# Kernel optimization log

Hardware: AMD Instinct MI355X
Metric: run time of the kernel (lower is better)

## Reference

```python
import jax, jax.numpy as jnp
from jax import lax
import numpy as np

# H=W=16 is forced by the module: mask path is a fixed 4x4 lowres map -> ConvTranspose(stride 4) -> 16x16
B, T, H, W = 512, 18, 16, 16
CH, K, D = 128, 8, 128


def setup_inputs():
    key = jax.random.key(0)
    ks = iter(jax.random.split(key, 40))
    def rn(shape, s=0.1):
        return jax.random.normal(next(ks), shape, jnp.float32) * s
    return dict(
        frames=jax.random.uniform(next(ks), (B, T, 1, H, W), jnp.float32),
        enc1_w=rn((CH, 2, 3, 3)), enc1_b=rn((CH,)),
        enc2_w=rn((CH, CH, 4, 4), 0.02), enc2_b=rn((CH,)),
        slot_mu=rn((1, K, D), 0.1),
        to_slot_w=rn((D, CH)), to_slot_b=rn((D,)),
        q_w=rn((D, D)), k_w=rn((D, D)), v_w=rn((D, D)),
        gru_w_ih=rn((3 * D, D)), gru_w_hh=rn((3 * D, D)),
        gru_b_ih=rn((3 * D,)), gru_b_hh=rn((3 * D,)),
        mot1_w=rn((32, D)), mot1_b=rn((32,)),
        mot2_w=rn((2, 32)), mot2_b=rn((2,)),
        mask_w=rn((CH * 16, D)), mask_b=rn((CH * 16,)),
        up_w=rn((K, K, 4, 4)), up_b=rn((K,)),
        res1_w=rn((CH // 2, 1, 3, 3)), res1_b=rn((CH // 2,)),
        res2_w=rn((1, CH // 2, 3, 3)), res2_b=rn((1,)),
    )


def _conv(x, w, b, stride, pad):
    y = lax.conv_general_dilated(x, w, (stride, stride), [(pad, pad), (pad, pad)],
                                 dimension_numbers=('NCHW', 'OIHW', 'NCHW'))
    return y + b[None, :, None, None]


def _gelu(x):
    return jax.nn.gelu(x, approximate=False)  # torch nn.GELU default = exact erf


def reference(frames, enc1_w, enc1_b, enc2_w, enc2_b, slot_mu, to_slot_w, to_slot_b,
              q_w, k_w, v_w, gru_w_ih, gru_w_hh, gru_b_ih, gru_b_hh,
              mot1_w, mot1_b, mot2_w, mot2_b, mask_w, mask_b, up_w, up_b,
              res1_w, res1_b, res2_w, res2_b):
    Bq, Tq = frames.shape[0], frames.shape[1]
    Hh, Ww = frames.shape[-2], frames.shape[-1]
    Kq, Dq = slot_mu.shape[1], slot_mu.shape[2]
    scale = Dq ** 0.5
    # base sampling grid in normalized [-1,1] coords, order (x, y)
    gy, gx = jnp.meshgrid(jnp.linspace(-1.0, 1.0, Hh), jnp.linspace(-1.0, 1.0, Ww), indexing='ij')
    grid = jnp.stack([gx, gy], axis=-1)  # [H,W,2]
    # ConvTranspose2d weight [in,out,kh,kw] -> equivalent forward-conv kernel (swap io, flip spatial)
    up_w_f = jnp.flip(up_w, (2, 3)).transpose(1, 0, 2, 3)

    def gru(x, h):  # torch nn.GRUCell, gate order r,z,n
        gi = x @ gru_w_ih.T + gru_b_ih
        gh = h @ gru_w_hh.T + gru_b_hh
        ir, iz, inn = jnp.split(gi, 3, axis=-1)
        hr, hz, hn = jnp.split(gh, 3, axis=-1)
        r = jax.nn.sigmoid(ir + hr)
        z = jax.nn.sigmoid(iz + hz)
        n = jnp.tanh(inn + r * hn)
        return (1.0 - z) * n + z * h

    def step(slots, pair):
        curr = pair[:, :1]  # [B,1,H,W]
        feat = _gelu(_conv(pair, enc1_w, enc1_b, 1, 1))
        feat = _gelu(_conv(feat, enc2_w, enc2_b, 4, 0))  # [B,CH,H/4,W/4]
        fs = jnp.einsum('bcn,dc->bnd', feat.reshape(Bq, feat.shape[1], -1), to_slot_w) + to_slot_b
        kk = fs @ k_w.T
        vv = fs @ v_w.T
        for _ in range(3):  # fixed 3 slot-attention iterations
            qq = slots @ q_w.T
            attn = jax.nn.softmax(jnp.einsum('bkd,bnd->bkn', qq, kk) / scale, axis=1)
            upd = jnp.einsum('bkn,bnd->bkd', attn, vv)
            slots = gru(upd.reshape(-1, Dq), slots.reshape(-1, Dq)).reshape(Bq, Kq, Dq)
        motion = jnp.tanh(_gelu(slots @ mot1_w.T + mot1_b) @ mot2_w.T + mot2_b) * 4.0  # [B,K,2]
        ml = (slots @ mask_w.T + mask_b).reshape(Bq, Kq, -1, 4, 4).mean(axis=2)  # [B,K,4,4]
        masks = lax.conv_general_dilated(ml, up_w_f, (1, 1), [(3, 3), (3, 3)],
                                         lhs_dilation=(4, 4),
                                         dimension_numbers=('NCHW', 'OIHW', 'NCHW')) + up_b[None, :, None, None]
        masks = jax.nn.softmax(masks, axis=1)  # [B,K,16,16]
        # batched per-slot warp (constant translation per slot); grid_sample bilinear,
        # border padding, align_corners=True
        fsc = motion * 2.0 / jnp.array([Ww, Hh], jnp.float32)
        sg = jnp.clip(grid[None, None] + fsc[:, :, None, None, :], -1.0, 1.0)  # [B,K,H,W,2]
        ix = (sg[..., 0] + 1.0) * 0.5 * (Ww - 1)
        iy = (sg[..., 1] + 1.0) * 0.5 * (Hh - 1)
        x0 = jnp.floor(ix); y0 = jnp.floor(iy)
        wx = ix - x0; wy = iy - y0
        x0i = jnp.clip(x0, 0, Ww - 1).astype(jnp.int32)
        x1i = jnp.clip(x0 + 1, 0, Ww - 1).astype(jnp.int32)
        y0i = jnp.clip(y0, 0, Hh - 1).astype(jnp.int32)
        y1i = jnp.clip(y0 + 1, 0, Hh - 1).astype(jnp.int32)
        img = curr[:, 0]  # [B,H,W]
        bidx = jnp.arange(Bq)[:, None, None, None]
        v00 = img[bidx, y0i, x0i]; v01 = img[bidx, y0i, x1i]
        v10 = img[bidx, y1i, x0i]; v11 = img[bidx, y1i, x1i]
        warped_k = (1 - wy) * ((1 - wx) * v00 + wx * v01) + wy * ((1 - wx) * v10 + wx * v11)  # [B,K,H,W]
        warped = (masks * warped_k).sum(axis=1, keepdims=True)  # [B,1,H,W]
        res = jnp.tanh(_conv(_gelu(_conv(warped - curr, res1_w, res1_b, 1, 1)), res2_w, res2_b, 1, 1)) * 0.1
        pred = jnp.clip(warped + res, 0.0, 1.0)
        return slots, pred

    slots0 = jnp.broadcast_to(slot_mu, (Bq, Kq, Dq))
    # pair = cat([curr, prev], dim=1) for t in 0..T-3
    pairs = jnp.swapaxes(jnp.concatenate([frames[:, 1:Tq - 1], frames[:, :Tq - 2]], axis=2), 0, 1)
    _, preds = lax.scan(step, slots0, pairs)
    return jnp.swapaxes(preds, 0, 1)  # [B,T-2,1,H,W]
```

## Files before the change

kernel.cpp:

```cpp
#include <hip/hip_runtime.h>
#include <math.h>

#define B_TOT 512
#define T_FR  18
#define NSTEP 16

typedef __attribute__((ext_vector_type(8))) short bf16x8;
typedef __attribute__((ext_vector_type(4))) float f32x4;

__device__ __forceinline__ float gelu_f(float x) {
    return 0.5f * x * (1.0f + erff(x * 0.70710678118654752f));
}
__device__ __forceinline__ float sigmoid_f(float x) {
    return 1.0f / (1.0f + expf(-x));
}
__device__ __forceinline__ short f2bf(float x) {
    unsigned int u = __float_as_uint(x);
    return (short)((u + 0x7FFFu + ((u >> 16) & 1u)) >> 16);
}
__device__ __forceinline__ float bflo(unsigned int u) { return __uint_as_float(u << 16); }
__device__ __forceinline__ float bfhi(unsigned int u) { return __uint_as_float(u & 0xffff0000u); }
__device__ __forceinline__ float bf2f(short s) {
    return __uint_as_float(((unsigned int)(unsigned short)s) << 16);
}
__device__ __forceinline__ bf16x8 ld_bf8(const short* p) {
    const short4 lo = *reinterpret_cast<const short4*>(p);
    const short4 hi = *reinterpret_cast<const short4*>(p + 4);
    bf16x8 r;
    r[0] = lo.x; r[1] = lo.y; r[2] = lo.z; r[3] = lo.w;
    r[4] = hi.x; r[5] = hi.y; r[6] = hi.z; r[7] = hi.w;
    return r;
}

#define MFMA(a, bb, c) __builtin_amdgcn_mfma_f32_16x16x32_bf16((a), (bb), (c), 0, 0, 0)

__global__ __launch_bounds__(256) void init_kernel(
    const float* __restrict__ mask_w, const float* __restrict__ mask_b,
    const float* __restrict__ e2w,
    const float* __restrict__ wih, const float* __restrict__ whh,
    const float* __restrict__ qw,
    const float* __restrict__ tsw, const float* __restrict__ tsb,
    const float* __restrict__ kw, const float* __restrict__ vw,
    const float* __restrict__ e1w, const float* __restrict__ e1b,
    float* __restrict__ rmw, float* __restrict__ rmb,
    float* __restrict__ kbf, float* __restrict__ vbf,
    short* __restrict__ w2bf, short* __restrict__ wihbf, short* __restrict__ whhbf,
    short* __restrict__ qwbf, short* __restrict__ kwf, short* __restrict__ vwf,
    short* __restrict__ e1wbf)
{
    const int tid = threadIdx.x, bid = blockIdx.x;
    const int gid = bid * 256 + tid, gstr = gridDim.x * 256;
    const float rscale = 0.08838834764831845f;

    for (int i = gid; i < 128 * 2048; i += gstr) w2bf[i] = f2bf(e2w[i]);
    for (int i = gid; i < 384 * 128; i += gstr) {
        wihbf[i] = f2bf(wih[i]);
        whhbf[i] = f2bf(whh[i]);
    }
    for (int i = gid; i < 128 * 128; i += gstr) qwbf[i] = f2bf(qw[i] * rscale);
    for (int i = gid; i < 128 * 32; i += gstr) {
        const int ci = i >> 5, k = i & 31;
        float v = 0.f;
        if (k < 18) v = e1w[ci * 18 + k];
        else if (k == 18) v = e1b[ci];
        e1wbf[i] = f2bf(v);
    }

    if (bid < 128) {
        const int j = bid;
        if (tid < 128) {
            float s = 0.f;
            for (int d = 0; d < 128; ++d) s += kw[j * 128 + d] * tsw[d * 128 + tid];
            kwf[j * 128 + tid] = f2bf(s);
        } else if (tid == 128) {
            float s = 0.f;
            for (int d = 0; d < 128; ++d) s += kw[j * 128 + d] * tsb[d];
            kbf[j] = s;
        }
    } else if (bid < 256) {
        const int j = bid - 128;
        if (tid < 128) {
            float s = 0.f;
            for (int d = 0; d < 128; ++d) s += vw[j * 128 + d] * tsw[d * 128 + tid];
            vwf[j * 128 + tid] = f2bf(s);
        } else if (tid == 128) {
            float s = 0.f;
            for (int d = 0; d < 128; ++d) s += vw[j * 128 + d] * tsb[d];
            vbf[j] = s;
        }
    }
    if (bid == 256) {
        for (int i = tid; i < 2048; i += 256) {
            const int j = i >> 7, d = i & 127;
            float s = 0.f;
            for (int c = 0; c < 128; ++c) s += mask_w[(c * 16 + j) * 128 + d];
            rmw[i] = s * (1.0f / 128.0f);
        }
        for (int i = tid; i < 16; i += 256) {
            float s = 0.f;
            for (int c = 0; c < 128; ++c) s += mask_b[c * 16 + i];
            rmb[i] = s * (1.0f / 128.0f);
        }
    }
}

#define E_PAIR 0
#define E_IM2C 2048
#define E_F1S  20480
#define E_F2T  40960
#define E_E2B  45184
#define E_KBF  45696
#define E_VBF  46208
#define EPOOLSZ 46720

__global__ __launch_bounds__(256, 2) void encoder_all_kernel(
    const float* __restrict__ frames,
    const short* __restrict__ w2bf, const short* __restrict__ e1wbf,
    const float* __restrict__ e2b_g,
    const short* __restrict__ kwf, const short* __restrict__ vwf,
    const float* __restrict__ kbf_g, const float* __restrict__ vbf_g,
    short* __restrict__ kk_g, short* __restrict__ vv_g)
{
    __shared__ __align__(16) char POOL[EPOOLSZ];
    float* PAIR = (float*)(POOL + E_PAIR);
    short* IM2C = (short*)(POOL + E_IM2C);
    short* F1S  = (short*)(POOL + E_F1S);
    short* F2T  = (short*)(POOL + E_F2T);
    float* E2B  = (float*)(POOL + E_E2B);
    float* KBF  = (float*)(POOL + E_KBF);
    float* VBF  = (float*)(POOL + E_VBF);

    const int tid = threadIdx.x;
    const int lane = tid & 63, w = tid >> 6;
    const int g = lane >> 4, cn = lane & 15;
    const int bid = blockIdx.x;
    const int b = bid >> 4, t = bid & 15;
    const int py = tid >> 4, pxx = tid & 15;
    const int arow = (2 * w) * 16 + cn;
    const int bcol = (4 * (cn >> 2) + (g & 1) * 2) * 20 + 4 * (cn & 3);

    PAIR[tid]       = frames[((size_t)b * T_FR + t + 1) * 256 + tid];
    PAIR[256 + tid] = frames[((size_t)b * T_FR + t) * 256 + tid];
    if (tid < 128) {
        E2B[tid] = e2b_g[tid];
        KBF[tid] = kbf_g[tid];
        VBF[tid] = vbf_g[tid];
    }
    __syncthreads();

    {
        short* imr = &IM2C[tid * 36];
#pragma unroll
        for (int ky = 0; ky < 3; ++ky)
#pragma unroll
        for (int kx = 0; kx < 3; ++kx) {
            const int yy = py + ky - 1, xx = pxx + kx - 1;
            const bool ok = (yy >= 0 && yy < 16 && xx >= 0 && xx < 16);
            const int q = ky * 3 + kx;
            imr[q]     = ok ? f2bf(PAIR[yy * 16 + xx]) : (short)0;
            imr[9 + q] = ok ? f2bf(PAIR[256 + yy * 16 + xx]) : (short)0;
        }
        imr[18] = (short)0x3F80;
        imr[19] = 0;
        short4 z4; z4.x = 0; z4.y = 0; z4.z = 0; z4.w = 0;
        *(short4*)&imr[20] = z4;
        *(short4*)&imr[24] = z4;
        *(short4*)&imr[28] = z4;
    }
    __syncthreads();

    f32x4 acc0 = {0.f, 0.f, 0.f, 0.f};
    f32x4 acc1 = {0.f, 0.f, 0.f, 0.f};
    for (int ch = 0; ch < 4; ++ch) {
        {
            const bf16x8 aw0 = *(const bf16x8*)&e1wbf[(size_t)(ch * 32 + cn) * 32 + g * 8];
            const bf16x8 aw1 = *(const bf16x8*)&e1wbf[(size_t)(ch * 32 + 16 + cn) * 32 + g * 8];
            f32x4 c0[4], c1[4];
#pragma unroll
            for (int j = 0; j < 4; ++j) {
                c0[j] = (f32x4){0.f, 0.f, 0.f, 0.f};
                c1[j] = (f32x4){0.f, 0.f, 0.f, 0.f};
            }
#pragma unroll
            for (int j = 0; j < 4; ++j) {
                const int pos = (4 * w + j) * 16 + cn;
                const bf16x8 bim = ld_bf8(&IM2C[pos * 36 + g * 8]);
                c0[j] = MFMA(aw0, bim, c0[j]);
                c1[j] = MFMA(aw1, bim, c1[j]);
            }
#pragma unroll
            for (int j = 0; j < 4; ++j)
#pragma unroll
            for (int r = 0; r < 4; ++r) {
                F1S[(4 * g + r) * 320 + (4 * w + j) * 20 + cn] = f2bf(gelu_f(c0[j][r]));
                F1S[(16 + 4 * g + r) * 320 + (4 * w + j) * 20 + cn] = f2bf(gelu_f(c1[j][r]));
            }
        }
        __syncthreads();
        int rb = (g >> 1) * 320 + bcol;
        int k0 = ch * 512 + g * 8;
        for (int kt = 0; kt < 16; ++kt) {
            const short4 lo = *(const short4*)&F1S[rb];
            const short4 hi = *(const short4*)&F1S[rb + 20];
            bf16x8 bfr;
            bfr[0] = lo.x; bfr[1] = lo.y; bfr[2] = lo.z; bfr[3] = lo.w;
            bfr[4] = hi.x; bfr[5] = hi.y; bfr[6] = hi.z; bfr[7] = hi.w;
            const bf16x8 a0 = *(const bf16x8*)&w2bf[(size_t)arow * 2048 + k0];
            const bf16x8 a1 = *(const bf16x8*)&w2bf[(size_t)(arow + 16) * 2048 + k0];
            acc0 = MFMA(a0, bfr, acc0);
            acc1 = MFMA(a1, bfr, acc1);
            rb += 640; k0 += 32;
        }
        __syncthreads();
    }
    {
        const int cob0 = (2 * w) * 16 + g * 4;
        short4 s0, s1;
        s0.x = f2bf(gelu_f(acc0[0] + E2B[cob0]));
        s0.y = f2bf(gelu_f(acc0[1] + E2B[cob0 + 1]));
        s0.z = f2bf(gelu_f(acc0[2] + E2B[cob0 + 2]));
        s0.w = f2bf(gelu_f(acc0[3] + E2B[cob0 + 3]));
        s1.x = f2bf(gelu_f(acc1[0] + E2B[cob0 + 16]));
        s1.y = f2bf(gelu_f(acc1[1] + E2B[cob0 + 17]));
        s1.z = f2bf(gelu_f(acc1[2] + E2B[cob0 + 18]));
        s1.w = f2bf(gelu_f(acc1[3] + E2B[cob0 + 19]));
        *(short4*)&F2T[cn * 132 + cob0] = s0;
        *(short4*)&F2T[cn * 132 + cob0 + 16] = s1;
    }
    __syncthreads();

    {
        bf16x8 aT[4];
#pragma unroll
        for (int kt = 0; kt < 4; ++kt)
            aT[kt] = ld_bf8(&F2T[cn * 132 + kt * 32 + g * 8]);
        const short* wf = (w >> 1) ? vwf : kwf;
        const int h2 = w & 1;
        f32x4 ac[4];
#pragma unroll
        for (int nt = 0; nt < 4; ++nt) ac[nt] = (f32x4){0.f, 0.f, 0.f, 0.f};
#pragma unroll
        for (int kt = 0; kt < 4; ++kt)
#pragma unroll
        for (int nt = 0; nt < 4; ++nt)
            ac[nt] = MFMA(aT[kt],
                *(const bf16x8*)&wf[(size_t)(h2 * 64 + nt * 16 + cn) * 128 + kt * 32 + g * 8],
                ac[nt]);
        short* dst = (w >> 1) ? vv_g : kk_g;
        const float* bias = (w >> 1) ? VBF : KBF;
        const size_t base = (size_t)bid * 2048;
#pragma unroll
        for (int nt = 0; nt < 4; ++nt) {
            const int j = h2 * 64 + nt * 16 + cn;
            const float bb = bias[j];
#pragma unroll
            for (int r = 0; r < 4; ++r)
                dst[base + (4 * g + r) * 128 + j] = f2bf(ac[nt][r] + bb);
        }
    }
}

#define PO_BIH   0
#define PO_BHH   1536
#define PO_M1B   3072
#define PO_M2W   3200
#define PO_M2B   3456
#define PO_UPB   3472
#define PO_RMB   3504
#define PO_R2B   3568
#define PO_UPW   3584
#define PO_R1W   7680
#define PO_R1B   9984
#define PO_R2W   10240
#define PO_M1W   12544
#define PO_RMW   20992
#define PO_SLOTS 25216
#define PO_SLB   29312
#define SCR2     33536
#define T_KK   0
#define T_VV   4224
#define T_QQ   8448
#define T_UPD  12672
#define T_ATT  16896
#define T_MASK 0
#define T_IMG  8192
#define T_WARP 9216
#define T_DIFF 10240
#define T_M1O  11264
#define T_MOT  12288
#define T_MLL  12416
#define T_R1S  12928
#define POOLSZ2 (33536 + 21376)

#define LDW(mat, row, kt) (*(const bf16x8*)&mat[(size_t)(row) * 128 + (kt) * 32 + g * 8])

__global__ __launch_bounds__(256, 2) void fused_seq_kernel(
    const float* __restrict__ frames,
    const float* __restrict__ slot_mu,
    const short* __restrict__ kk_g, const short* __restrict__ vv_g,
    const short* __restrict__ qwbf,
    const short* __restrict__ wihbf, const short* __restrict__ whhbf,
    const float* __restrict__ bih_g, const float* __restrict__ bhh_g,
    const float* __restrict__ m1w_g, const float* __restrict__ m1b_g,
    const float* __restrict__ m2w_g, const float* __restrict__ m2b_g,
    const float* __restrict__ upw_g, const float* __restrict__ upb_g,
    const float* __restrict__ r1w_g, const float* __restrict__ r1b_g,
    const float* __restrict__ r2w_g, const float* __restrict__ r2b_g,
    const float* __restrict__ rmw_g, const float* __restrict__ rmb_g,
    float* __restrict__ out)
{
    __shared__ __align__(16) char POOL[POOLSZ2];
    const int tid = threadIdx.x;
    const int lane = tid & 63, w = tid >> 6;
    const int g = lane >> 4, cn = lane & 15;
    const int b = blockIdx.x;

    float* BIH = (float*)(POOL + PO_BIH);
    float* BHH = (float*)(POOL + PO_BHH);
    float* M1B = (float*)(POOL + PO_M1B);
    float* M2W = (float*)(POOL + PO_M2W);
    float* M2B = (float*)(POOL + PO_M2B);
    float* UPB = (float*)(POOL + PO_UPB);
    float* RMB = (float*)(POOL + PO_RMB);
    float* R2B = (float*)(POOL + PO_R2B);
    float* UPW = (float*)(POOL + PO_UPW);
    float* R1W = (float*)(POOL + PO_R1W);
    float* R1B = (float*)(POOL + PO_R1B);
    float* R2W = (float*)(POOL + PO_R2W);
    short* M1W = (short*)(POOL + PO_M1W);
    short* RMW = (short*)(POOL + PO_RMW);
    float* SLOTS = (float*)(POOL + PO_SLOTS);
    short* SLB = (short*)(POOL + PO_SLB);

    short* KKl  = (short*)(POOL + SCR2 + T_KK);
    short* VVl  = (short*)(POOL + SCR2 + T_VV);
    short* QQB  = (short*)(POOL + SCR2 + T_QQ);
    short* UPDB = (short*)(POOL + SCR2 + T_UPD);
    float* ATT  = (float*)(POOL + SCR2 + T_ATT);
    float* MASKl = (float*)(POOL + SCR2 + T_MASK);
    float* IMG  = (float*)(POOL + SCR2 + T_IMG);
    float* WARP = (float*)(POOL + SCR2 + T_WARP);
    float* DIFF = (float*)(POOL + SCR2 + T_DIFF);
    float* M1O  = (float*)(POOL + SCR2 + T_M1O);
    float* MOT  = (float*)(POOL + SCR2 + T_MOT);
    float* MLL  = (float*)(POOL + SCR2 + T_MLL);
    short* R1S  = (short*)(POOL + SCR2 + T_R1S);

    for (int i = tid; i < 384; i += 256) { BIH[i] = bih_g[i]; BHH[i] = bhh_g[i]; }
    if (tid < 32) M1B[tid] = m1b_g[tid];
    if (tid < 64) { M2W[tid] = m2w_g[tid]; R1B[tid] = r1b_g[tid]; }
    if (tid < 2) M2B[tid] = m2b_g[tid];
    if (tid < 8) UPB[tid] = upb_g[tid];
    if (tid < 16) RMB[tid] = rmb_g[tid];
    if (tid == 0) R2B[0] = r2b_g[0];
    for (int i = tid; i < 1024; i += 256) UPW[i] = upw_g[i];
    for (int i = tid; i < 576; i += 256) { R1W[i] = r1w_g[i]; R2W[i] = r2w_g[i]; }
    for (int i = tid; i < 4096; i += 256)
        M1W[(i >> 7) * 132 + (i & 127)] = f2bf(m1w_g[i]);
    for (int i = tid; i < 2048; i += 256)
        RMW[(i >> 7) * 132 + (i & 127)] = f2bf(rmw_g[i]);
    for (int i = tid; i < 1024; i += 256) {
        const float v = slot_mu[i];
        SLOTS[i] = v;
        SLB[(i >> 7) * 132 + (i & 127)] = f2bf(v);
    }
    for (int i = tid; i < 8 * 132; i += 256) SLB[8 * 132 + i] = 0;

    const int col0 = 32 * w;
    const int py = tid >> 4, pxx = tid & 15;
    __syncthreads();

#pragma unroll 1
    for (int t = 0; t < NSTEP; ++t) {
        const float imgv = frames[((size_t)b * T_FR + t + 1) * 256 + tid];

        {
            const size_t base = ((size_t)b * 16 + t) * 2048;
            const int row = tid >> 4, c8 = (tid & 15) * 8;
            const short4 klo = *(const short4*)&kk_g[base + row * 128 + c8];
            const short4 khi = *(const short4*)&kk_g[base + row * 128 + c8 + 4];
            const short4 vlo = *(const short4*)&vv_g[base + row * 128 + c8];
            const short4 vhi = *(const short4*)&vv_g[base + row * 128 + c8 + 4];
            *(short4*)&KKl[row * 132 + c8] = klo;
            *(short4*)&KKl[row * 132 + c8 + 4] = khi;
            *(short4*)&VVl[row * 132 + c8] = vlo;
            *(short4*)&VVl[row * 132 + c8 + 4] = vhi;
        }
        __syncthreads();

        for (int it = 0; it < 3; ++it) {
            bf16x8 aS[4];
#pragma unroll
            for (int kt = 0; kt < 4; ++kt)
                aS[kt] = ld_bf8(&SLB[cn * 132 + kt * 32 + g * 8]);
            {
                f32x4 qa[2] = {{0.f, 0.f, 0.f, 0.f}, {0.f, 0.f, 0.f, 0.f}};
#pragma unroll
                for (int kt = 0; kt < 4; ++kt)
#pragma unroll
                for (int nt = 0; nt < 2; ++nt)
                    qa[nt] = MFMA(aS[kt], LDW(qwbf, col0 + nt * 16 + cn, kt), qa[nt]);
#pragma unroll
                for (int nt = 0; nt < 2; ++nt)
#pragma unroll
                for (int r = 0; r < 4; ++r)
                    QQB[(4 * g + r) * 132 + col0 + nt * 16 + cn] = f2bf(qa[nt][r]);
            }
            __syncthreads();
            if (tid < 128) {
                const int n = tid >> 3, k = tid & 7;
                float a = 0.f;
                for (int d = 0; d < 128; d += 4) {
                    const uint2 q2 = *(const uint2*)&QQB[k * 132 + d];
                    const uint2 k2 = *(const uint2*)&KKl[n * 132 + d];
                    a += bflo(q2.x) * bflo(k2.x) + bfhi(q2.x) * bfhi(k2.x)
                       + bflo(q2.y) * bflo(k2.y) + bfhi(q2.y) * bfhi(k2.y);
                }
                float m = a;
                m = fmaxf(m, __shfl_xor(m, 1));
                m = fmaxf(m, __shfl_xor(m, 2));
                m = fmaxf(m, __shfl_xor(m, 4));
                const float e = expf(a - m);
                float s = e;
                s += __shfl_xor(s, 1);
                s += __shfl_xor(s, 2);
                s += __shfl_xor(s, 4);
                ATT[k * 16 + n] = e / s;
            }
            __syncthreads();
            {
                const int k8 = tid >> 5, lg = tid & 31;
                float a0 = 0.f, a1 = 0.f, a2 = 0.f, a3 = 0.f;
#pragma unroll
                for (int n = 0; n < 16; ++n) {
                    const float at = ATT[k8 * 16 + n];
                    const uint2 v2 = *(const uint2*)&VVl[n * 132 + 4 * lg];
                    a0 += at * bflo(v2.x); a1 += at * bfhi(v2.x);
                    a2 += at * bflo(v2.y); a3 += at * bfhi(v2.y);
                }
                short4 sv;
                sv.x = f2bf(a0); sv.y = f2bf(a1); sv.z = f2bf(a2); sv.w = f2bf(a3);
                *(short4*)&UPDB[k8 * 132 + 4 * lg] = sv;
            }
            __syncthreads();
            {
                bf16x8 aU[4];
#pragma unroll
                for (int kt = 0; kt < 4; ++kt)
                    aU[kt] = ld_bf8(&UPDB[cn * 132 + kt * 32 + g * 8]);
                f32x4 aR[2], aZ[2], aNIv[2], aNHv[2];
#pragma unroll
                for (int nt = 0; nt < 2; ++nt) {
                    aR[nt] = (f32x4){0.f, 0.f, 0.f, 0.f};
                    aZ[nt] = (f32x4){0.f, 0.f, 0.f, 0.f};
                    aNIv[nt] = (f32x4){0.f, 0.f, 0.f, 0.f};
                    aNHv[nt] = (f32x4){0.f, 0.f, 0.f, 0.f};
                }
#pragma unroll
                for (int nt = 0; nt < 2; ++nt) {
                    const int colj = col0 + nt * 16 + cn;
#pragma unroll
                    for (int kt = 0; kt < 4; ++kt) {
                        aR[nt]   = MFMA(aU[kt], LDW(wihbf, colj, kt), aR[nt]);
                        aR[nt]   = MFMA(aS[kt], LDW(whhbf, colj, kt), aR[nt]);
                        aZ[nt]   = MFMA(aU[kt], LDW(wihbf, 128 + colj, kt), aZ[nt]);
                        aZ[nt]   = MFMA(aS[kt], LDW(whhbf, 128 + colj, kt), aZ[nt]);
                        aNIv[nt] = MFMA(aU[kt], LDW(wihbf, 256 + colj, kt), aNIv[nt]);
                        aNHv[nt] = MFMA(aS[kt], LDW(whhbf, 256 + colj, kt), aNHv[nt]);
                    }
                }
                __syncthreads();
                if (g < 2) {
#pragma unroll
                    for (int nt = 0; nt < 2; ++nt) {
                        const int colj = col0 + nt * 16 + cn;
                        const float br = BIH[colj] + BHH[colj];
                        const float bz = BIH[128 + colj] + BHH[128 + colj];
                        const float bi = BIH[256 + colj], bh = BHH[256 + colj];
#pragma unroll
                        for (int r = 0; r < 4; ++r) {
                            const int kq = 4 * g + r;
                            const float rr = sigmoid_f(aR[nt][r] + br);
                            const float zz = sigmoid_f(aZ[nt][r] + bz);
                            const float nn = tanhf(aNIv[nt][r] + bi + rr * (aNHv[nt][r] + bh));
                            const float hold = SLOTS[kq * 128 + colj];
                            const float hv = (1.f - zz) * nn + zz * hold;
                            SLOTS[kq * 128 + colj] = hv;
                            SLB[kq * 132 + colj] = f2bf(hv);
                        }
                    }
                }
                __syncthreads();
            }
        }

        IMG[tid] = imgv;
        {
            const int kq = tid >> 5, c = tid & 31;
            float a = M1B[c];
            for (int d = 0; d < 128; d += 4) {
                const uint2 s2 = *(const uint2*)&SLB[kq * 132 + d];
                const uint2 w2 = *(const uint2*)&M1W[c * 132 + d];
                a += bflo(s2.x) * bflo(w2.x) + bfhi(s2.x) * bfhi(w2.x)
                   + bflo(s2.y) * bflo(w2.y) + bfhi(s2.y) * bfhi(w2.y);
            }
            M1O[kq * 32 + c] = gelu_f(a);
        }
        if (tid < 128) {
            const int kq = tid >> 4, j = tid & 15;
            float a = RMB[j];
            for (int d = 0; d < 128; d += 4) {
                const uint2 s2 = *(const uint2*)&SLB[kq * 132 + d];
                const uint2 w2 = *(const uint2*)&RMW[j * 132 + d];
                a += bflo(s2.x) * bflo(w2.x) + bfhi(s2.x) * bfhi(w2.x)
                   + bflo(s2.y) * bflo(w2.y) + bfhi(s2.y) * bfhi(w2.y);
            }
            MLL[kq * 16 + j] = a;
        }
        __syncthreads();
        if (tid < 16) {
            const int kq = tid >> 1, e = tid & 1;
            float a = M2B[e];
#pragma unroll
            for (int c = 0; c < 32; ++c) a += M1O[kq * 32 + c] * M2W[e * 32 + c];
            MOT[kq * 2 + e] = tanhf(a) * 4.0f;
        }
        {
            const int jj = (py >> 2) * 4 + (pxx >> 2);
            const int wq = (py & 3) * 4 + (pxx & 3);
#pragma unroll
            for (int ko = 0; ko < 8; ++ko) {
                float a = UPB[ko];
#pragma unroll
                for (int i8 = 0; i8 < 8; ++i8)
                    a += MLL[i8 * 16 + jj] * UPW[(i8 * 8 + ko) * 16 + wq];
                MASKl[ko * 256 + tid] = a;
            }
        }
        __syncthreads();
        {
            float m = -1e30f;
#pragma unroll
            for (int kq = 0; kq < 8; ++kq) m = fmaxf(m, MASKl[kq * 256 + tid]);
            float e[8], ssum = 0.f;
#pragma unroll
            for (int kq = 0; kq < 8; ++kq) { e[kq] = expf(MASKl[kq * 256 + tid] - m); ssum += e[kq]; }
            const float inv = 1.f / ssum;
            const float gxv = -1.0f + (2.0f / 15.0f) * pxx;
            const float gyv = -1.0f + (2.0f / 15.0f) * py;
            float wsum = 0.f;
#pragma unroll
            for (int kq = 0; kq < 8; ++kq) {
                const float fx = MOT[kq * 2 + 0] * 0.125f;
                const float fy = MOT[kq * 2 + 1] * 0.125f;
                const float sgx = fminf(fmaxf(gxv + fx, -1.f), 1.f);
                const float sgy = fminf(fmaxf(gyv + fy, -1.f), 1.f);
                const float ix = (sgx + 1.f) * 7.5f;
                const float iy = (sgy + 1.f) * 7.5f;
                const float x0f = floorf(ix), y0f = floorf(iy);
                const float wx = ix - x0f, wy = iy - y0f;
                const int x0 = (int)x0f, y0 = (int)y0f;
                const int x1 = min(x0 + 1, 15), y1 = min(y0 + 1, 15);
                const float v00 = IMG[y0 * 16 + x0], v01 = IMG[y0 * 16 + x1];
                const float v10 = IMG[y1 * 16 + x0], v11 = IMG[y1 * 16 + x1];
                const float val = (1.f - wy) * ((1.f - wx) * v00 + wx * v01) +
                                  wy * ((1.f - wx) * v10 + wx * v11);
                wsum += (e[kq] * inv) * val;
            }
            WARP[tid] = wsum;
            DIFF[tid] = wsum - IMG[tid];
        }
        __syncthreads();
        float nbz[9];
#pragma unroll
        for (int ky = 0; ky < 3; ++ky)
#pragma unroll
        for (int kx = 0; kx < 3; ++kx) {
            const int y2 = py + ky - 1, x2 = pxx + kx - 1;
            const bool ok = (y2 >= 0 && y2 < 16 && x2 >= 0 && x2 < 16);
            nbz[ky * 3 + kx] = ok ? DIFF[y2 * 16 + x2] : 0.f;
        }
        float racc = 0.f;
        for (int c0 = 0; c0 < 64; c0 += 16) {
#pragma unroll 4
            for (int cl = 0; cl < 16; ++cl) {
                const int c = c0 + cl;
                float a = R1B[c];
#pragma unroll
                for (int q = 0; q < 9; ++q) a += nbz[q] * R1W[c * 9 + q];
                R1S[cl * 264 + tid] = f2bf(gelu_f(a));
            }
            __syncthreads();
#pragma unroll 4
            for (int cl = 0; cl < 16; ++cl) {
                const float* r2r = &R2W[(c0 + cl) * 9];
#pragma unroll
                for (int ky = 0; ky < 3; ++ky)
#pragma unroll
                for (int kx = 0; kx < 3; ++kx) {
                    const int y2 = py + ky - 1, x2 = pxx + kx - 1;
                    if (y2 >= 0 && y2 < 16 && x2 >= 0 && x2 < 16)
                        racc += bf2f(R1S[cl * 264 + y2 * 16 + x2]) * r2r[ky * 3 + kx];
                }
            }
            __syncthreads();
        }
        const float resv = tanhf(racc + R2B[0]) * 0.1f;
        const float pred = fminf(fmaxf(WARP[tid] + resv, 0.f), 1.f);
        out[((size_t)b * NSTEP + t) * 256 + tid] = pred;
        __syncthreads();
    }
}

extern "C" void kernel_launch(void* const* d_in, const int* in_sizes, int n_in,
                              void* d_out, int out_size, void* d_ws, size_t ws_size,
                              hipStream_t stream)
{
    const float* frames = (const float*)d_in[0];
    const float* e1w = (const float*)d_in[1];
    const float* e1b = (const float*)d_in[2];
    const float* e2w = (const float*)d_in[3];
    const float* e2b = (const float*)d_in[4];
    const float* slot_mu = (const float*)d_in[5];
    const float* tsw = (const float*)d_in[6];
    const float* tsb = (const float*)d_in[7];
    const float* qw = (const float*)d_in[8];
    const float* kw = (const float*)d_in[9];
    const float* vw = (const float*)d_in[10];
    const float* wih = (const float*)d_in[11];
    const float* whh = (const float*)d_in[12];
    const float* bih = (const float*)d_in[13];
    const float* bhh = (const float*)d_in[14];
    const float* m1w = (const float*)d_in[15];
    const float* m1b = (const float*)d_in[16];
    const float* m2w = (const float*)d_in[17];
    const float* m2b = (const float*)d_in[18];
    const float* maskw = (const float*)d_in[19];
    const float* maskb = (const float*)d_in[20];
    const float* upw = (const float*)d_in[21];
    const float* upb = (const float*)d_in[22];
    const float* r1w = (const float*)d_in[23];
    const float* r1b = (const float*)d_in[24];
    const float* r2w = (const float*)d_in[25];
    const float* r2b = (const float*)d_in[26];

    float* ws = (float*)d_ws;
    float* rmw  = ws + 0;
    float* rmb  = ws + 2048;
    float* kbf  = ws + 2064;
    float* vbf  = ws + 2192;
    short* w2bf  = (short*)(ws + 2320);
    short* wihbf = (short*)(ws + 133392);
    short* whhbf = (short*)(ws + 157968);
    short* qwbf  = (short*)(ws + 182544);
    short* kwf   = (short*)(ws + 190736);
    short* vwf   = (short*)(ws + 198928);
    short* e1wbf = (short*)(ws + 207120);
    short* kk_g  = (short*)(ws + 209168);
    short* vv_g  = (short*)(ws + 209168 + 8388608);

    hipLaunchKernelGGL(init_kernel, dim3(512), dim3(256), 0, stream,
                       maskw, maskb, e2w, wih, whh, qw, tsw, tsb, kw, vw,
                       e1w, e1b,
                       rmw, rmb, kbf, vbf, w2bf, wihbf, whhbf, qwbf, kwf, vwf,
                       e1wbf);
    hipLaunchKernelGGL(encoder_all_kernel, dim3(B_TOT * NSTEP), dim3(256), 0, stream,
                       frames, w2bf, e1wbf, e2b, kwf, vwf, kbf, vbf, kk_g, vv_g);
    hipLaunchKernelGGL(fused_seq_kernel, dim3(B_TOT), dim3(256), 0, stream,
                       frames, slot_mu, kk_g, vv_g, qwbf, wihbf, whhbf, bih, bhh,
                       m1w, m1b, m2w, m2b, upw, upb,
                       r1w, r1b, r2w, r2b, rmw, rmb,
                       (float*)d_out);
}
```

Before: 1.803 ms.

## Split per-step decoder out of sequential slot kernel into parallel decode kernel

The slot recurrence kernel no longer runs the motion/mask/warp/residual decoder inside its time loop. It writes the updated slots for each step into the kk_g buffer, overwriting the K values already consumed for that step. A new kernel with one block per (batch, step) then runs the decoder, so decode work no longer sits on the 512-block sequential critical path and its shared memory leaves the recurrent kernel, which may allow more occupancy. The cost is an extra launch, a global round trip of the slots, and reloading the decoder weights in every one of 8192 blocks.

```diff
diff --git a/kernel.cpp b/kernel.cpp
--- a/kernel.cpp
+++ b/kernel.cpp
@@ -262,52 +262,24 @@
 
 #define PO_BIH   0
 #define PO_BHH   1536
-#define PO_M1B   3072
-#define PO_M2W   3200
-#define PO_M2B   3456
-#define PO_UPB   3472
-#define PO_RMB   3504
-#define PO_R2B   3568
-#define PO_UPW   3584
-#define PO_R1W   7680
-#define PO_R1B   9984
-#define PO_R2W   10240
-#define PO_M1W   12544
-#define PO_RMW   20992
-#define PO_SLOTS 25216
-#define PO_SLB   29312
-#define SCR2     33536
+#define PO_SLOTS 3072
+#define PO_SLB   7168
+#define SCR2     11392
 #define T_KK   0
 #define T_VV   4224
 #define T_QQ   8448
 #define T_UPD  12672
 #define T_ATT  16896
-#define T_MASK 0
-#define T_IMG  8192
-#define T_WARP 9216
-#define T_DIFF 10240
-#define T_M1O  11264
-#define T_MOT  12288
-#define T_MLL  12416
-#define T_R1S  12928
-#define POOLSZ2 (33536 + 21376)
+#define POOLSZ2 (11392 + 17408)
 
 #define LDW(mat, row, kt) (*(const bf16x8*)&mat[(size_t)(row) * 128 + (kt) * 32 + g * 8])
 
 __global__ __launch_bounds__(256, 2) void fused_seq_kernel(
-    const float* __restrict__ frames,
     const float* __restrict__ slot_mu,
-    const short* __restrict__ kk_g, const short* __restrict__ vv_g,
+    short* __restrict__ kk_g, const short* __restrict__ vv_g,
     const short* __restrict__ qwbf,
     const short* __restrict__ wihbf, const short* __restrict__ whhbf,
-    const float* __restrict__ bih_g, const float* __restrict__ bhh_g,
-    const float* __restrict__ m1w_g, const float* __restrict__ m1b_g,
-    const float* __restrict__ m2w_g, const float* __restrict__ m2b_g,
-    const float* __restrict__ upw_g, const float* __restrict__ upb_g,
-    const float* __restrict__ r1w_g, const float* __restrict__ r1b_g,
-    const float* __restrict__ r2w_g, const float* __restrict__ r2b_g,
-    const float* __restrict__ rmw_g, const float* __restrict__ rmb_g,
-    float* __restrict__ out)
+    const float* __restrict__ bih_g, const float* __restrict__ bhh_g)
 {
     __shared__ __align__(16) char POOL[POOLSZ2];
     const int tid = threadIdx.x;
@@ -317,18 +289,6 @@
 
     float* BIH = (float*)(POOL + PO_BIH);
     float* BHH = (float*)(POOL + PO_BHH);
-    float* M1B = (float*)(POOL + PO_M1B);
-    float* M2W = (float*)(POOL + PO_M2W);
-    float* M2B = (float*)(POOL + PO_M2B);
-    float* UPB = (float*)(POOL + PO_UPB);
-    float* RMB = (float*)(POOL + PO_RMB);
-    float* R2B = (float*)(POOL + PO_R2B);
-    float* UPW = (float*)(POOL + PO_UPW);
-    float* R1W = (float*)(POOL + PO_R1W);
-    float* R1B = (float*)(POOL + PO_R1B);
-    float* R2W = (float*)(POOL + PO_R2W);
-    short* M1W = (short*)(POOL + PO_M1W);
-    short* RMW = (short*)(POOL + PO_RMW);
     float* SLOTS = (float*)(POOL + PO_SLOTS);
     short* SLB = (short*)(POOL + PO_SLB);
 
@@ -337,28 +297,8 @@
     short* QQB  = (short*)(POOL + SCR2 + T_QQ);
     short* UPDB = (short*)(POOL + SCR2 + T_UPD);
     float* ATT  = (float*)(POOL + SCR2 + T_ATT);
-    float* MASKl = (float*)(POOL + SCR2 + T_MASK);
-    float* IMG  = (float*)(POOL + SCR2 + T_IMG);
-    float* WARP = (float*)(POOL + SCR2 + T_WARP);
-    float* DIFF = (float*)(POOL + SCR2 + T_DIFF);
-    float* M1O  = (float*)(POOL + SCR2 + T_M1O);
-    float* MOT  = (float*)(POOL + SCR2 + T_MOT);
-    float* MLL  = (float*)(POOL + SCR2 + T_MLL);
-    short* R1S  = (short*)(POOL + SCR2 + T_R1S);
 
     for (int i = tid; i < 384; i += 256) { BIH[i] = bih_g[i]; BHH[i] = bhh_g[i]; }
-    if (tid < 32) M1B[tid] = m1b_g[tid];
-    if (tid < 64) { M2W[tid] = m2w_g[tid]; R1B[tid] = r1b_g[tid]; }
-    if (tid < 2) M2B[tid] = m2b_g[tid];
-    if (tid < 8) UPB[tid] = upb_g[tid];
-    if (tid < 16) RMB[tid] = rmb_g[tid];
-    if (tid == 0) R2B[0] = r2b_g[0];
-    for (int i = tid; i < 1024; i += 256) UPW[i] = upw_g[i];
-    for (int i = tid; i < 576; i += 256) { R1W[i] = r1w_g[i]; R2W[i] = r2w_g[i]; }
-    for (int i = tid; i < 4096; i += 256)
-        M1W[(i >> 7) * 132 + (i & 127)] = f2bf(m1w_g[i]);
-    for (int i = tid; i < 2048; i += 256)
-        RMW[(i >> 7) * 132 + (i & 127)] = f2bf(rmw_g[i]);
     for (int i = tid; i < 1024; i += 256) {
         const float v = slot_mu[i];
         SLOTS[i] = v;
@@ -367,13 +307,10 @@
     for (int i = tid; i < 8 * 132; i += 256) SLB[8 * 132 + i] = 0;
 
     const int col0 = 32 * w;
-    const int py = tid >> 4, pxx = tid & 15;
     __syncthreads();
 
 #pragma unroll 1
     for (int t = 0; t < NSTEP; ++t) {
-        const float imgv = frames[((size_t)b * T_FR + t + 1) * 256 + tid];
-
         {
             const size_t base = ((size_t)b * 16 + t) * 2048;
             const int row = tid >> 4, c8 = (tid & 15) * 8;
@@ -494,122 +431,212 @@
             }
         }
 
-        IMG[tid] = imgv;
         {
-            const int kq = tid >> 5, c = tid & 31;
-            float a = M1B[c];
-            for (int d = 0; d < 128; d += 4) {
-                const uint2 s2 = *(const uint2*)&SLB[kq * 132 + d];
-                const uint2 w2 = *(const uint2*)&M1W[c * 132 + d];
-                a += bflo(s2.x) * bflo(w2.x) + bfhi(s2.x) * bfhi(w2.x)
-                   + bflo(s2.y) * bflo(w2.y) + bfhi(s2.y) * bfhi(w2.y);
+            const size_t base = ((size_t)b * 16 + t) * 2048;
+            const int i4 = tid * 4;
+            const int row = i4 >> 7, col = i4 & 127;
+            *(short4*)&kk_g[base + i4] = *(const short4*)&SLB[row * 132 + col];
+        }
+        __syncthreads();
+    }
+}
+
+#define D_SLB  0
+#define D_M1W  2112
+#define D_RMW  10560
+#define D_UPW  14784
+#define D_R1W  18880
+#define D_R2W  21184
+#define D_M1B  23488
+#define D_M2W  23616
+#define D_M2B  23872
+#define D_UPB  23888
+#define D_RMB  23920
+#define D_R2B  23984
+#define D_R1B  24000
+#define D_IMG  24256
+#define D_MASK 25280
+#define D_WARP 33472
+#define D_DIFF 34496
+#define D_M1O  35520
+#define D_MOT  36544
+#define D_MLL  36672
+#define D_R1S  37184
+#define POOLSZ3 45632
+
+__global__ __launch_bounds__(256, 2) void decode_all_kernel(
+    const float* __restrict__ frames,
+    const short* __restrict__ slots_g,
+    const float* __restrict__ m1w_g, const float* __restrict__ m1b_g,
+    const float* __restrict__ m2w_g, const float* __restrict__ m2b_g,
+    const float* __restrict__ upw_g, const float* __restrict__ upb_g,
+    const float* __restrict__ r1w_g, const float* __restrict__ r1b_g,
+    const float* __restrict__ r2w_g, const float* __restrict__ r2b_g,
+    const float* __restrict__ rmw_g, const float* __restrict__ rmb_g,
+    float* __restrict__ out)
+{
+    __shared__ __align__(16) char POOL[POOLSZ3];
+    short* SLB = (short*)(POOL + D_SLB);
+    short* M1W = (short*)(POOL + D_M1W);
+    short* RMW = (short*)(POOL + D_RMW);
+    float* UPW = (float*)(POOL + D_UPW);
+    float* R1W = (float*)(POOL + D_R1W);
+    float* R2W = (float*)(POOL + D_R2W);
+    float* M1B = (float*)(POOL + D_M1B);
+    float* M2W = (float*)(POOL + D_M2W);
+    float* M2B = (float*)(POOL + D_M2B);
+    float* UPB = (float*)(POOL + D_UPB);
+    float* RMB = (float*)(POOL + D_RMB);
+    float* R2B = (float*)(POOL + D_R2B);
+    float* R1B = (float*)(POOL + D_R1B);
+    float* IMG = (float*)(POOL + D_IMG);
+    float* MASKl = (float*)(POOL + D_MASK);
+    float* WARP = (float*)(POOL + D_WARP);
+    float* DIFF = (float*)(POOL + D_DIFF);
+    float* M1O  = (float*)(POOL + D_M1O);
+    float* MOT  = (float*)(POOL + D_MOT);
+    float* MLL  = (float*)(POOL + D_MLL);
+    short* R1S  = (short*)(POOL + D_R1S);
+
+    const int tid = threadIdx.x;
+    const int bid = blockIdx.x;
+    const int b = bid >> 4, t = bid & 15;
+    const int py = tid >> 4, pxx = tid & 15;
+
+    {
+        const size_t base = (size_t)bid * 2048;
+        const int i4 = tid * 4;
+        const int row = i4 >> 7, col = i4 & 127;
+        *(short4*)&SLB[row * 132 + col] = *(const short4*)&slots_g[base + i4];
+    }
+    for (int i = tid; i < 4096; i += 256)
+        M1W[(i >> 7) * 132 + (i & 127)] = f2bf(m1w_g[i]);
+    for (int i = tid; i < 2048; i += 256)
+        RMW[(i >> 7) * 132 + (i & 127)] = f2bf(rmw_g[i]);
+    for (int i = tid; i < 1024; i += 256) UPW[i] = upw_g[i];
+    for (int i = tid; i < 576; i += 256) { R1W[i] = r1w_g[i]; R2W[i] = r2w_g[i]; }
+    if (tid < 32) M1B[tid] = m1b_g[tid];
+    if (tid < 64) { M2W[tid] = m2w_g[tid]; R1B[tid] = r1b_g[tid]; }
+    if (tid < 2) M2B[tid] = m2b_g[tid];
+    if (tid < 8) UPB[tid] = upb_g[tid];
+    if (tid < 16) RMB[tid] = rmb_g[tid];
+    if (tid == 0) R2B[0] = r2b_g[0];
+    IMG[tid] = frames[((size_t)b * T_FR + t + 1) * 256 + tid];
+    __syncthreads();
+
+    {
+        const int kq = tid >> 5, c = tid & 31;
+        float a = M1B[c];
+        for (int d = 0; d < 128; d += 4) {
+            const uint2 s2 = *(const uint2*)&SLB[kq * 132 + d];
+            const uint2 w2 = *(const uint2*)&M1W[c * 132 + d];
+            a += bflo(s2.x) * bflo(w2.x) + bfhi(s2.x) * bfhi(w2.x)
+               + bflo(s2.y) * bflo(w2.y) + bfhi(s2.y) * bfhi(w2.y);
+        }
+        M1O[kq * 32 + c] = gelu_f(a);
+    }
+    if (tid < 128) {
+        const int kq = tid >> 4, j = tid & 15;
+        float a = RMB[j];
+        for (int d = 0; d < 128; d += 4) {
+            const uint2 s2 = *(const uint2*)&SLB[kq * 132 + d];
+            const uint2 w2 = *(const uint2*)&RMW[j * 132 + d];
+            a += bflo(s2.x) * bflo(w2.x) + bfhi(s2.x) * bfhi(w2.x)
+               + bflo(s2.y) * bflo(w2.y) + bfhi(s2.y) * bfhi(w2.y);
+        }
+        MLL[kq * 16 + j] = a;
+    }
+    __syncthreads();
+    if (tid < 16) {
+        const int kq = tid >> 1, e = tid & 1;
+        float a = M2B[e];
+#pragma unroll
+        for (int c = 0; c < 32; ++c) a += M1O[kq * 32 + c] * M2W[e * 32 + c];
+        MOT[kq * 2 + e] = tanhf(a) * 4.0f;
+    }
+    {
+        const int jj = (py >> 2) * 4 + (pxx >> 2);
+        const int wq = (py & 3) * 4 + (pxx & 3);
+#pragma unroll
+        for (int ko = 0; ko < 8; ++ko) {
+            float a = UPB[ko];
+#pragma unroll
+            for (int i8 = 0; i8 < 8; ++i8)
+                a += MLL[i8 * 16 + jj] * UPW[(i8 * 8 + ko) * 16 + wq];
+            MASKl[ko * 256 + tid] = a;
+        }
+    }
+    __syncthreads();
+    {
+        float m = -1e30f;
+#pragma unroll
+        for (int kq = 0; kq < 8; ++kq) m = fmaxf(m, MASKl[kq * 256 + tid]);
+        float e[8], ssum = 0.f;
+#pragma unroll
+        for (int kq = 0; kq < 8; ++kq) { e[kq] = expf(MASKl[kq * 256 + tid] - m); ssum += e[kq]; }
+        const float inv = 1.f / ssum;
+        const float gxv = -1.0f + (2.0f / 15.0f) * pxx;
+        const float gyv = -1.0f + (2.0f / 15.0f) * py;
+        float wsum = 0.f;
+#pragma unroll
+        for (int kq = 0; kq < 8; ++kq) {
+            const float fx = MOT[kq * 2 + 0] * 0.125f;
+            const float fy = MOT[kq * 2 + 1] * 0.125f;
+            const float sgx = fminf(fmaxf(gxv + fx, -1.f), 1.f);
+            const float sgy = fminf(fmaxf(gyv + fy, -1.f), 1.f);
+            const float ix = (sgx + 1.f) * 7.5f;
+            const float iy = (sgy + 1.f) * 7.5f;
+            const float x0f = floorf(ix), y0f = floorf(iy);
+            const float wx = ix - x0f, wy = iy - y0f;
+            const int x0 = (int)x0f, y0 = (int)y0f;
+            const int x1 = min(x0 + 1, 15), y1 = min(y0 + 1, 15);
+            const float v00 = IMG[y0 * 16 + x0], v01 = IMG[y0 * 16 + x1];
+            const float v10 = IMG[y1 * 16 + x0], v11 = IMG[y1 * 16 + x1];
+            const float val = (1.f - wy) * ((1.f - wx) * v00 + wx * v01) +
+                              wy * ((1.f - wx) * v10 + wx * v11);
+            wsum += (e[kq] * inv) * val;
+        }
+        WARP[tid] = wsum;
+        DIFF[tid] = wsum - IMG[tid];
+    }
+    __syncthreads();
+    float nbz[9];
+#pragma unroll
+    for (int ky = 0; ky < 3; ++ky)
+#pragma unroll
+    for (int kx = 0; kx < 3; ++kx) {
+        const int y2 = py + ky - 1, x2 = pxx + kx - 1;
+        const bool ok = (y2 >= 0 && y2 < 16 && x2 >= 0 && x2 < 16);
+        nbz[ky * 3 + kx] = ok ? DIFF[y2 * 16 + x2] : 0.f;
+    }
+    float racc = 0.f;
+    for (int c0 = 0; c0 < 64; c0 += 16) {
+#pragma unroll 4
+        for (int cl = 0; cl < 16; ++cl) {
+            const int c = c0 + cl;
+            float a = R1B[c];
+#pragma unroll
+            for (int q = 0; q < 9; ++q) a += nbz[q] * R1W[c * 9 + q];
+            R1S[cl * 264 + tid] = f2bf(gelu_f(a));
+        }
+        __syncthreads();
+#pragma unroll 4
+        for (int cl = 0; cl < 16; ++cl) {
+            const float* r2r = &R2W[(c0 + cl) * 9];
+#pragma unroll
+            for (int ky = 0; ky < 3; ++ky)
+#pragma unroll
+            for (int kx = 0; kx < 3; ++kx) {
+                const int y2 = py + ky - 1, x2 = pxx + kx - 1;
+                if (y2 >= 0 && y2 < 16 && x2 >= 0 && x2 < 16)
+                    racc += bf2f(R1S[cl * 264 + y2 * 16 + x2]) * r2r[ky * 3 + kx];
             }
-            M1O[kq * 32 + c] = gelu_f(a);
-        }
-        if (tid < 128) {
-            const int kq = tid >> 4, j = tid & 15;
-            float a = RMB[j];
-            for (int d = 0; d < 128; d += 4) {
-                const uint2 s2 = *(const uint2*)&SLB[kq * 132 + d];
-                const uint2 w2 = *(const uint2*)&RMW[j * 132 + d];
-                a += bflo(s2.x) * bflo(w2.x) + bfhi(s2.x) * bfhi(w2.x)
-                   + bflo(s2.y) * bflo(w2.y) + bfhi(s2.y) * bfhi(w2.y);
-            }
-            MLL[kq * 16 + j] = a;
         }
         __syncthreads();
-        if (tid < 16) {
-            const int kq = tid >> 1, e = tid & 1;
-            float a = M2B[e];
-#pragma unroll
-            for (int c = 0; c < 32; ++c) a += M1O[kq * 32 + c] * M2W[e * 32 + c];
-            MOT[kq * 2 + e] = tanhf(a) * 4.0f;
-        }
-        {
-            const int jj = (py >> 2) * 4 + (pxx >> 2);
-            const int wq = (py & 3) * 4 + (pxx & 3);
-#pragma unroll
-            for (int ko = 0; ko < 8; ++ko) {
-                float a = UPB[ko];
-#pragma unroll
-                for (int i8 = 0; i8 < 8; ++i8)
-                    a += MLL[i8 * 16 + jj] * UPW[(i8 * 8 + ko) * 16 + wq];
-                MASKl[ko * 256 + tid] = a;
-            }
-        }
-        __syncthreads();
-        {
-            float m = -1e30f;
-#pragma unroll
-            for (int kq = 0; kq < 8; ++kq) m = fmaxf(m, MASKl[kq * 256 + tid]);
-            float e[8], ssum = 0.f;
-#pragma unroll
-            for (int kq = 0; kq < 8; ++kq) { e[kq] = expf(MASKl[kq * 256 + tid] - m); ssum += e[kq]; }
-            const float inv = 1.f / ssum;
-            const float gxv = -1.0f + (2.0f / 15.0f) * pxx;
-            const float gyv = -1.0f + (2.0f / 15.0f) * py;
-            float wsum = 0.f;
-#pragma unroll
-            for (int kq = 0; kq < 8; ++kq) {
-                const float fx = MOT[kq * 2 + 0] * 0.125f;
-                const float fy = MOT[kq * 2 + 1] * 0.125f;
-                const float sgx = fminf(fmaxf(gxv + fx, -1.f), 1.f);
-                const float sgy = fminf(fmaxf(gyv + fy, -1.f), 1.f);
-                const float ix = (sgx + 1.f) * 7.5f;
-                const float iy = (sgy + 1.f) * 7.5f;
-                const float x0f = floorf(ix), y0f = floorf(iy);
-                const float wx = ix - x0f, wy = iy - y0f;
-                const int x0 = (int)x0f, y0 = (int)y0f;
-                const int x1 = min(x0 + 1, 15), y1 = min(y0 + 1, 15);
-                const float v00 = IMG[y0 * 16 + x0], v01 = IMG[y0 * 16 + x1];
-                const float v10 = IMG[y1 * 16 + x0], v11 = IMG[y1 * 16 + x1];
-                const float val = (1.f - wy) * ((1.f - wx) * v00 + wx * v01) +
-                                  wy * ((1.f - wx) * v10 + wx * v11);
-                wsum += (e[kq] * inv) * val;
-            }
-            WARP[tid] = wsum;
-            DIFF[tid] = wsum - IMG[tid];
-        }
-        __syncthreads();
-        float nbz[9];
-#pragma unroll
-        for (int ky = 0; ky < 3; ++ky)
-#pragma unroll
-        for (int kx = 0; kx < 3; ++kx) {
-            const int y2 = py + ky - 1, x2 = pxx + kx - 1;
-            const bool ok = (y2 >= 0 && y2 < 16 && x2 >= 0 && x2 < 16);
-            nbz[ky * 3 + kx] = ok ? DIFF[y2 * 16 + x2] : 0.f;
-        }
-        float racc = 0.f;
-        for (int c0 = 0; c0 < 64; c0 += 16) {
-#pragma unroll 4
-            for (int cl = 0; cl < 16; ++cl) {
-                const int c = c0 + cl;
-                float a = R1B[c];
-#pragma unroll
-                for (int q = 0; q < 9; ++q) a += nbz[q] * R1W[c * 9 + q];
-                R1S[cl * 264 + tid] = f2bf(gelu_f(a));
-            }
-            __syncthreads();
-#pragma unroll 4
-            for (int cl = 0; cl < 16; ++cl) {
-                const float* r2r = &R2W[(c0 + cl) * 9];
-#pragma unroll
-                for (int ky = 0; ky < 3; ++ky)
-#pragma unroll
-                for (int kx = 0; kx < 3; ++kx) {
-                    const int y2 = py + ky - 1, x2 = pxx + kx - 1;
-                    if (y2 >= 0 && y2 < 16 && x2 >= 0 && x2 < 16)
-                        racc += bf2f(R1S[cl * 264 + y2 * 16 + x2]) * r2r[ky * 3 + kx];
-                }
-            }
-            __syncthreads();
-        }
-        const float resv = tanhf(racc + R2B[0]) * 0.1f;
-        const float pred = fminf(fmaxf(WARP[tid] + resv, 0.f), 1.f);
-        out[((size_t)b * NSTEP + t) * 256 + tid] = pred;
-        __syncthreads();
-    }
+    }
+    const float resv = tanhf(racc + R2B[0]) * 0.1f;
+    const float pred = fminf(fmaxf(WARP[tid] + resv, 0.f), 1.f);
+    out[((size_t)b * NSTEP + t) * 256 + tid] = pred;
 }
 
 extern "C" void kernel_launch(void* const* d_in, const int* in_sizes, int n_in,
@@ -667,8 +694,9 @@
     hipLaunchKernelGGL(encoder_all_kernel, dim3(B_TOT * NSTEP), dim3(256), 0, stream,
                        frames, w2bf, e1wbf, e2b, kwf, vwf, kbf, vbf, kk_g, vv_g);
     hipLaunchKernelGGL(fused_seq_kernel, dim3(B_TOT), dim3(256), 0, stream,
-                       frames, slot_mu, kk_g, vv_g, qwbf, wihbf, whhbf, bih, bhh,
-                       m1w, m1b, m2w, m2b, upw, upb,
+                       slot_mu, kk_g, vv_g, qwbf, wihbf, whhbf, bih, bhh);
+    hipLaunchKernelGGL(decode_all_kernel, dim3(B_TOT * NSTEP), dim3(256), 0, stream,
+                       frames, kk_g, m1w, m1b, m2w, m2b, upw, upb,
                        r1w, r1b, r2w, r2b, rmw, rmb,
                        (float*)d_out);
 }
```

After: 1.558 ms, median of 2. 13.6% less time.
